# Kernel tuning notes

Hardware: AMD Instinct MI355X
Metric: run time of the kernel (lower is better)

The kernel has to match this reference:

```python
import jax, jax.numpy as jnp
import numpy as np

B, N, IN_DIM, ATT_DIM = 2, 8192, 512, 512


def setup_inputs() -> dict:
    key = jax.random.key(0)
    k1, k2, k3, k4 = jax.random.split(key, 4)
    X = jax.random.normal(k1, (B, N, IN_DIM), dtype=jnp.float32)
    adj = jax.random.uniform(k2, (B, N, N), dtype=jnp.float32)
    mask = jnp.ones((B, N), dtype=jnp.float32)
    # Learned params (torch Linear stores W as (out,in); we store (in,out) for x @ W)
    Wqk = jax.random.normal(k3, (IN_DIM, 2 * ATT_DIM), dtype=jnp.float32) / np.sqrt(IN_DIM)
    Wv = jax.random.normal(k4, (IN_DIM, IN_DIM), dtype=jnp.float32) / np.sqrt(IN_DIM)
    return {"X": X, "adj": adj, "mask": mask, "Wqk": Wqk, "Wv": Wv}


def reference(X, adj, mask, Wqk, Wv):
    # q, k: (B, N, att_dim); v: (B, N, in_dim)
    qk = X @ Wqk
    q, k = jnp.split(qk, 2, axis=-1)
    v = X @ Wv
    att_dim = q.shape[-1]
    inv_scale = 1.0 / jnp.sqrt(jnp.float32(att_dim))
    # Original math: w_i = inv_scale * sum_j adj_ij * m_i * m_j * (q_i . k_j).
    # Since the rank-1 mask factors (m_i m_j), fold m_j into k and m_i into the row
    # score, avoiding a second materialized NxN tensor:
    k_m = k * mask[:, :, None]                       # (B, N, att_dim)
    agg = jnp.einsum("bij,bjd->bid", adj, k_m)       # (B, N, att_dim)
    w = inv_scale * mask * jnp.einsum("bid,bid->bi", q, agg)  # (B, N)
    # softmax over the bag dimension (dim=1), then scale v rows
    L = jax.nn.softmax(w, axis=1)[:, :, None] * v    # (B, N, in_dim)
    return L
```

## Files before the change

kernel.cpp:

```cpp
#include <hip/hip_runtime.h>
#include <math.h>

#define BB 2
#define NN 8192
#define DD 512

static const float INV_SCALE = 0.04419417382415922f;

typedef short s16x8 __attribute__((ext_vector_type(8)));
typedef unsigned short u16x8 __attribute__((ext_vector_type(8)));
typedef float f32x4 __attribute__((ext_vector_type(4)));

#define AS1 __attribute__((address_space(1)))
#define AS3 __attribute__((address_space(3)))

__device__ __forceinline__ unsigned short bfbits(__bf16 h) {
    return __builtin_bit_cast(unsigned short, h);
}

__device__ __forceinline__ void gll16(const void* g, void* l) {
    __builtin_amdgcn_global_load_lds((const AS1 unsigned int*)g, (AS3 unsigned int*)l, 16, 0, 0);
}

__global__ __launch_bounds__(256) void convx_k(
    const float* __restrict__ X, unsigned short* __restrict__ Xhi,
    unsigned short* __restrict__ Xlo)
{
    long i = (long)blockIdx.x * 256 + threadIdx.x;
    float4 x = ((const float4*)X)[i];
    __bf16 h0 = (__bf16)x.x, h1 = (__bf16)x.y, h2 = (__bf16)x.z, h3 = (__bf16)x.w;
    ushort4 hi4 = make_ushort4(bfbits(h0), bfbits(h1), bfbits(h2), bfbits(h3));
    __bf16 l0 = (__bf16)(x.x - (float)h0), l1 = (__bf16)(x.y - (float)h1);
    __bf16 l2 = (__bf16)(x.z - (float)h2), l3 = (__bf16)(x.w - (float)h3);
    ushort4 lo4 = make_ushort4(bfbits(l0), bfbits(l1), bfbits(l2), bfbits(l3));
    ((ushort4*)Xhi)[i] = hi4;
    ((ushort4*)Xlo)[i] = lo4;
}

__global__ __launch_bounds__(256) void convw_k(
    const float* __restrict__ Wqk, const float* __restrict__ Wv,
    unsigned short* __restrict__ QTh, unsigned short* __restrict__ QTl,
    unsigned short* __restrict__ VTh, unsigned short* __restrict__ VTl)
{
    int i = blockIdx.x * 256 + threadIdx.x;
    float val; unsigned short *ph, *pl;
    if (i < 524288) {
        int n = i >> 9, k = i & 511;
        val = Wqk[k * 1024 + n]; ph = QTh + i; pl = QTl + i;
    } else {
        int o = i - 524288; int n = o >> 9, k = o & 511;
        val = Wv[k * 512 + n]; ph = VTh + o; pl = VTl + o;
    }
    __bf16 h = (__bf16)val;
    __bf16 l = (__bf16)(val - (float)h);
    *ph = bfbits(h); *pl = bfbits(l);
}

template <int EPI, int NT>
__global__ __launch_bounds__(256, 2) void mfma_gemm(
    const unsigned short* __restrict__ A0, const unsigned short* __restrict__ A1,
    const unsigned short* __restrict__ B0, const unsigned short* __restrict__ B1,
    float* __restrict__ C,
    float* __restrict__ q, float* __restrict__ km,
    unsigned short* __restrict__ qh, unsigned short* __restrict__ kmh,
    const float* __restrict__ mask, int N, int K)
{
    constexpr int BK = 32;
    constexpr int TILE_SH = 128 * BK;

    __shared__ unsigned short Asm[2 * TILE_SH];
    __shared__ unsigned short Bsm[2 * TILE_SH];

    const int t = threadIdx.x;
    const int wv = t >> 6, lane = t & 63;
    const int wm = wv >> 1, wn = wv & 1;
    const long m0 = blockIdx.x * 128;
    const int n0 = blockIdx.y * 128;

    f32x4 acc[4][4];
#pragma unroll
    for (int i = 0; i < 4; ++i)
#pragma unroll
        for (int j = 0; j < 4; ++j) acc[i][j] = {0.f, 0.f, 0.f, 0.f};

    const int swzcol = ((lane & 3) ^ ((lane >> 2) & 3)) * 16;
    auto stageA16 = [&](int term, int k0, int buf) {
        const unsigned short* Ab = (term < 2) ? A0 : A1;
#pragma unroll
        for (int u = 0; u < 2; ++u) {
            int c = wv * 2 + u;
            int row = c * 16 + (lane >> 2);
            gll16((const char*)Ab + ((m0 + row) * (long)K + k0) * 2 + swzcol,
                  (char*)Asm + buf * (TILE_SH * 2) + c * 1024);
        }
    };
    auto stageB16 = [&](int term, int k0, int buf) {
        const unsigned short* Bb = (NT == 3 && term == 1) ? B1 : B0;
#pragma unroll
        for (int u = 0; u < 2; ++u) {
            int c = wv * 2 + u;
            int row = c * 16 + (lane >> 2);
            gll16((const char*)Bb + ((long)(n0 + row) * K + k0) * 2 + swzcol,
                  (char*)Bsm + buf * (TILE_SH * 2) + c * 1024);
        }
    };

    stageA16(0, 0, 0);
    stageB16(0, 0, 0);
    __syncthreads();

    const int NTILES = NT * (K / BK);
    int cur = 0, term = 0, k0 = 0;
    const int g = lane >> 4;

#pragma unroll 2
    for (int tt = 0; tt < NTILES; ++tt) {
        int k0n = k0 + BK, termn = term;
        if (k0n == K) { k0n = 0; ++termn; }
        const bool hasNext = (tt + 1 < NTILES);

        if (hasNext) {
            stageA16(termn, k0n, cur ^ 1);
            stageB16(termn, k0n, cur ^ 1);
        }

        s16x8 av[4], bv[4];
#pragma unroll
        for (int f = 0; f < 4; ++f) {
            int ra = wm * 64 + f * 16 + (lane & 15);
            int rb = wn * 64 + f * 16 + (lane & 15);
            av[f] = *(const s16x8*)(Asm + cur * TILE_SH + ra * BK + ((g ^ (ra & 3)) << 3));
            bv[f] = *(const s16x8*)(Bsm + cur * TILE_SH + rb * BK + ((g ^ (rb & 3)) << 3));
        }
#pragma unroll
        for (int fm = 0; fm < 4; ++fm)
#pragma unroll
            for (int fn = 0; fn < 4; ++fn)
                acc[fm][fn] = __builtin_amdgcn_mfma_f32_16x16x32_bf16(
                    av[fm], bv[fn], acc[fm][fn], 0, 0, 0);

        __syncthreads();
        cur ^= 1; term = termn; k0 = k0n;
    }

    const long rbase = m0 + wm * 64;
    const int cbase = n0 + wn * 64;

    if constexpr (EPI == 0) {
#pragma unroll
        for (int fm = 0; fm < 4; ++fm) {
            long rb = rbase + fm * 16 + ((lane >> 4) << 2);
#pragma unroll
            for (int fn = 0; fn < 4; ++fn) {
                int c = cbase + fn * 16 + (lane & 15);
#pragma unroll
                for (int j = 0; j < 4; ++j)
                    C[(rb + j) * (long)N + c] = acc[fm][fn][j];
            }
        }
    } else {
        const bool isq = (n0 < 512);
#pragma unroll
        for (int fm = 0; fm < 4; ++fm) {
            long rb = rbase + fm * 16 + ((lane >> 4) << 2);
#pragma unroll
            for (int fn = 0; fn < 4; ++fn) {
                int c = cbase + fn * 16 + (lane & 15);
                if (isq) {
#pragma unroll
                    for (int j = 0; j < 4; ++j) {
                        float val = acc[fm][fn][j];
                        q [(rb + j) * 512L + c] = val;
                        qh[(rb + j) * 512L + c] = bfbits((__bf16)val);
                    }
                } else {
                    int c2 = c - 512;
#pragma unroll
                    for (int j = 0; j < 4; ++j) {
                        float kv = acc[fm][fn][j] * mask[rb + j];
                        km [(rb + j) * 512L + c2] = kv;
                        kmh[(rb + j) * 512L + c2] = bfbits((__bf16)kv);
                    }
                }
            }
        }
    }
}

__global__ __launch_bounds__(256, 4) void sq_gemm(
    const unsigned short* __restrict__ qh,
    const unsigned short* __restrict__ kmh,
    const float* __restrict__ adj,
    float* __restrict__ w)
{
    constexpr int BK = 32;
    constexpr int TILE_SH = 128 * BK;

    __shared__ unsigned short Asm[2 * TILE_SH];
    __shared__ unsigned short Bsm[2 * TILE_SH];

    const int t = threadIdx.x;
    const int wv = t >> 6, lane = t & 63;
    const int wm = wv >> 1, wn = wv & 1;
    const int z = blockIdx.z;
    const long m0 = (long)z * NN + blockIdx.x * 128;
    const int n0 = blockIdx.y * 128;
    const unsigned short* Bz = kmh + (long)z * NN * 512;

    f32x4 acc[4][4];
#pragma unroll
    for (int i = 0; i < 4; ++i)
#pragma unroll
        for (int j = 0; j < 4; ++j) acc[i][j] = {0.f, 0.f, 0.f, 0.f};

    const int swzcol = ((lane & 3) ^ ((lane >> 2) & 3)) * 16;
    auto stageA = [&](int k0, int buf) {
#pragma unroll
        for (int u = 0; u < 2; ++u) {
            int c = wv * 2 + u;
            int row = c * 16 + (lane >> 2);
            gll16((const char*)qh + ((m0 + row) * 512L + k0) * 2 + swzcol,
                  (char*)Asm + buf * (TILE_SH * 2) + c * 1024);
        }
    };
    auto stageB = [&](int k0, int buf) {
#pragma unroll
        for (int u = 0; u < 2; ++u) {
            int c = wv * 2 + u;
            int row = c * 16 + (lane >> 2);
            gll16((const char*)Bz + ((long)(n0 + row) * 512 + k0) * 2 + swzcol,
                  (char*)Bsm + buf * (TILE_SH * 2) + c * 1024);
        }
    };

    stageA(0, 0);
    stageB(0, 0);
    __syncthreads();

    const int g = lane >> 4;
#pragma unroll 2
    for (int tt = 0; tt < 16; ++tt) {
        const int cur = tt & 1;
        const bool hasNext = (tt + 1 < 16);
        if (hasNext) {
            stageA((tt + 1) * BK, cur ^ 1);
            stageB((tt + 1) * BK, cur ^ 1);
        }

        s16x8 av[4], bv[4];
#pragma unroll
        for (int f = 0; f < 4; ++f) {
            int ra = wm * 64 + f * 16 + (lane & 15);
            int rb = wn * 64 + f * 16 + (lane & 15);
            av[f] = *(const s16x8*)(Asm + cur * TILE_SH + ra * BK + ((g ^ (ra & 3)) << 3));
            bv[f] = *(const s16x8*)(Bsm + cur * TILE_SH + rb * BK + ((g ^ (rb & 3)) << 3));
        }
#pragma unroll
        for (int fm = 0; fm < 4; ++fm)
#pragma unroll
            for (int fn = 0; fn < 4; ++fn)
                acc[fm][fn] = __builtin_amdgcn_mfma_f32_16x16x32_bf16(
                    av[fm], bv[fn], acc[fm][fn], 0, 0, 0);

        __syncthreads();
    }

    const float* adjZ = adj + (long)z * NN * NN;
    const int libase = blockIdx.x * 128 + wm * 64;
    const int jbase = n0 + wn * 64;
#pragma unroll
    for (int fm = 0; fm < 4; ++fm) {
#pragma unroll
        for (int j = 0; j < 4; ++j) {
            int li = libase + fm * 16 + ((lane >> 4) << 2) + j;
            const float* ar = adjZ + (long)li * NN + jbase + (lane & 15);
            float s = 0.f;
#pragma unroll
            for (int fn = 0; fn < 4; ++fn)
                s += ar[fn * 16] * acc[fm][fn][j];
            s += __shfl_xor(s, 1); s += __shfl_xor(s, 2);
            s += __shfl_xor(s, 4); s += __shfl_xor(s, 8);
            if ((lane & 15) == 0) atomicAdd(w + (long)z * NN + li, s);
        }
    }
}

__global__ __launch_bounds__(256) void fixup_k(
    float* __restrict__ w, const float* __restrict__ mask)
{
    int i = blockIdx.x * 256 + threadIdx.x;
    w[i] *= INV_SCALE * mask[i];
}

__global__ __launch_bounds__(256) void wmax_k(const float* __restrict__ w,
                                              float* __restrict__ wmax)
{
    const int b = blockIdx.x;
    const float* wr = w + (long)b * NN;
    const int t = threadIdx.x;
    float m = -3.4e38f;
    for (int i = t; i < NN; i += 256) m = fmaxf(m, wr[i]);
#pragma unroll
    for (int o = 32; o > 0; o >>= 1) m = fmaxf(m, __shfl_down(m, o));
    __shared__ float red[4];
    if ((t & 63) == 0) red[t >> 6] = m;
    __syncthreads();
    if (t == 0) wmax[b] = fmaxf(fmaxf(red[0], red[1]), fmaxf(red[2], red[3]));
}

__global__ __launch_bounds__(256) void select_k(
    const float* __restrict__ w, const float* __restrict__ wmax,
    int* __restrict__ count, int* __restrict__ cand)
{
    int i = blockIdx.x * 256 + threadIdx.x;
    int b = i >> 13;
    if (w[i] >= wmax[b] - 15.f) {
        int p = atomicAdd(count, 1);
        if (p < 128) cand[p] = i;
    }
}

__global__ __launch_bounds__(256) void refine_k(
    const float* __restrict__ q, const float* __restrict__ km,
    const float* __restrict__ adj, const int* __restrict__ cand,
    const int* __restrict__ count, float* __restrict__ partial)
{
    int y = blockIdx.y;
    int cnt = *count; if (cnt > 128) cnt = 128;
    if (y >= cnt) return;
    const int row = cand[y];
    const int b = row >> 13, r = row & 8191;
    const int x = blockIdx.x;
    const int t = threadIdx.x, w = t >> 6, l = t & 63;

    const float* qr = q + (long)row * 512 + l * 8;
    const float4 q0 = *(const float4*)qr;
    const float4 q1 = *(const float4*)(qr + 4);
    const float* kmB = km + ((long)b << 13) * 512;
    const float* adjR = adj + (((long)b << 13) + r) * 8192L;

    float acc = 0.f;
    const int jbase = x * 128 + w * 32;
    for (int i = 0; i < 32; ++i) {
        int j = jbase + i;
        const float* kr = kmB + (long)j * 512 + l * 8;
        const float4 k0 = *(const float4*)kr;
        const float4 k1 = *(const float4*)(kr + 4);
        float d = q0.x * k0.x + q0.y * k0.y + q0.z * k0.z + q0.w * k0.w
                + q1.x * k1.x + q1.y * k1.y + q1.z * k1.z + q1.w * k1.w;
#pragma unroll
        for (int o = 32; o > 0; o >>= 1) d += __shfl_down(d, o);
        if (l == 0) acc += adjR[j] * d;
    }
    __shared__ float red[4];
    if (l == 0) red[w] = acc;
    __syncthreads();
    if (t == 0) partial[y * 64 + x] = red[0] + red[1] + red[2] + red[3];
}

__global__ __launch_bounds__(128) void apply_k(
    const int* __restrict__ cand, const int* __restrict__ count,
    const float* __restrict__ partial, const float* __restrict__ mask,
    float* __restrict__ w)
{
    int t = threadIdx.x;
    int cnt = *count; if (cnt > 128) cnt = 128;
    if (t < cnt) {
        float s = 0.f;
        for (int x = 0; x < 64; ++x) s += partial[t * 64 + x];
        int row = cand[t];
        w[row] = s * INV_SCALE * mask[row];
    }
}

__global__ __launch_bounds__(1024) void softmax_k(
    const float* __restrict__ w, float* __restrict__ p)
{
    const int b = blockIdx.x;
    const float* wr = w + (long)b * NN;
    float* pr = p + (long)b * NN;
    const int t = threadIdx.x;
    __shared__ float red[16];
    __shared__ float bmax, bsum;

    float m = -3.4e38f;
    for (int i = t; i < NN; i += 1024) m = fmaxf(m, wr[i]);
#pragma unroll
    for (int o = 32; o > 0; o >>= 1) m = fmaxf(m, __shfl_down(m, o));
    if ((t & 63) == 0) red[t >> 6] = m;
    __syncthreads();
    if (t == 0) {
        float mm = red[0];
        for (int i = 1; i < 16; ++i) mm = fmaxf(mm, red[i]);
        bmax = mm;
    }
    __syncthreads();
    const float M = bmax;

    float s = 0.f;
    for (int i = t; i < NN; i += 1024) s += expf(wr[i] - M);
#pragma unroll
    for (int o = 32; o > 0; o >>= 1) s += __shfl_down(s, o);
    __syncthreads();
    if ((t & 63) == 0) red[t >> 6] = s;
    __syncthreads();
    if (t == 0) {
        float ss = 0.f;
        for (int i = 0; i < 16; ++i) ss += red[i];
        bsum = ss;
    }
    __syncthreads();
    const float invS = 1.f / bsum;
    for (int i = t; i < NN; i += 1024) pr[i] = expf(wr[i] - M) * invS;
}

__global__ __launch_bounds__(256) void scale_k(
    const float* __restrict__ v, const float* __restrict__ p,
    float* __restrict__ out)
{
    const long i = (long)blockIdx.x * 256 + threadIdx.x;
    const int row = (int)(i >> 7);
    const float pv = p[row];
    float4 vv = ((const float4*)v)[i];
    vv.x *= pv; vv.y *= pv; vv.z *= pv; vv.w *= pv;
    ((float4*)out)[i] = vv;
}

extern "C" void kernel_launch(void* const* d_in, const int* in_sizes, int n_in,
                              void* d_out, int out_size, void* d_ws, size_t ws_size,
                              hipStream_t stream)
{
    const float* X    = (const float*)d_in[0];
    const float* adj  = (const float*)d_in[1];
    const float* mask = (const float*)d_in[2];
    const float* Wqk  = (const float*)d_in[3];
    const float* Wv   = (const float*)d_in[4];
    float* out = (float*)d_out;

    char* ws = (char*)d_ws;
    const long SZB = 33554432;
    float* q_buf  = (float*)(ws);
    float* km_buf = (float*)(ws + SZB);
    float* v_buf  = (float*)(ws + 2 * SZB);
    unsigned short* Xhi = (unsigned short*)(ws + 3 * SZB);
    unsigned short* Xlo = Xhi + 8388608;
    unsigned short* qh  = (unsigned short*)(ws + 4 * SZB);
    unsigned short* kmh = qh + 8388608;
    unsigned short* QTh = kmh + 8388608;
    unsigned short* QTl = QTh + 524288;
    unsigned short* VTh = QTl + 524288;
    unsigned short* VTl = VTh + 262144;
    float* w_buf = (float*)(VTl + 262144);
    float* p_buf = w_buf + 16384;
    float* wmax  = p_buf + 16384;
    float* partial = wmax + 64;
    int* count = (int*)(partial + 8192);
    int* cand  = count + 64;

    hipMemsetAsync(count, 0, 4, stream);
    hipMemsetAsync(w_buf, 0, 16384 * 4, stream);

    convx_k<<<8192, 256, 0, stream>>>(X, Xhi, Xlo);
    convw_k<<<3072, 256, 0, stream>>>(Wqk, Wv, QTh, QTl, VTh, VTl);

    mfma_gemm<1, 3><<<dim3(128, 8, 1), 256, 0, stream>>>(
        Xhi, Xlo, QTh, QTl, nullptr, q_buf, km_buf, qh, kmh, mask, 1024, 512);

    mfma_gemm<0, 1><<<dim3(128, 4, 1), 256, 0, stream>>>(
        Xhi, nullptr, VTh, nullptr, v_buf, nullptr, nullptr, nullptr, nullptr,
        nullptr, 512, 512);

    sq_gemm<<<dim3(64, 64, 2), 256, 0, stream>>>(qh, kmh, adj, w_buf);

    fixup_k<<<64, 256, 0, stream>>>(w_buf, mask);

    wmax_k<<<BB, 256, 0, stream>>>(w_buf, wmax);
    select_k<<<64, 256, 0, stream>>>(w_buf, wmax, count, cand);
    refine_k<<<dim3(64, 128, 1), 256, 0, stream>>>(q_buf, km_buf, adj, cand, count, partial);
    apply_k<<<1, 128, 0, stream>>>(cand, count, partial, mask, w_buf);

    softmax_k<<<BB, 1024, 0, stream>>>(w_buf, p_buf);
    scale_k<<<8192, 256, 0, stream>>>(v_buf, p_buf, out);
}
```

Measured before the change: 463.3 us.

## Double GEMM K-tile to 64 with 8-way swizzle and XCD-aware block remap

```diff
diff --git a/kernel.cpp b/kernel.cpp
--- a/kernel.cpp
+++ b/kernel.cpp
@@ -56,6 +56,7 @@
     *ph = bfbits(h); *pl = bfbits(l);
 }
 
+
 template <int EPI, int NT>
 __global__ __launch_bounds__(256, 2) void mfma_gemm(
     const unsigned short* __restrict__ A0, const unsigned short* __restrict__ A1,
@@ -65,7 +66,7 @@
     unsigned short* __restrict__ qh, unsigned short* __restrict__ kmh,
     const float* __restrict__ mask, int N, int K)
 {
-    constexpr int BK = 32;
+    constexpr int BK = 64;
     constexpr int TILE_SH = 128 * BK;
 
     __shared__ unsigned short Asm[2 * TILE_SH];
@@ -83,30 +84,30 @@
 #pragma unroll
         for (int j = 0; j < 4; ++j) acc[i][j] = {0.f, 0.f, 0.f, 0.f};
 
-    const int swzcol = ((lane & 3) ^ ((lane >> 2) & 3)) * 16;
-    auto stageA16 = [&](int term, int k0, int buf) {
+    const int swz = ((lane & 7) ^ (lane >> 3)) << 4;
+    auto stageA = [&](int term, int k0, int buf) {
         const unsigned short* Ab = (term < 2) ? A0 : A1;
 #pragma unroll
-        for (int u = 0; u < 2; ++u) {
-            int c = wv * 2 + u;
-            int row = c * 16 + (lane >> 2);
-            gll16((const char*)Ab + ((m0 + row) * (long)K + k0) * 2 + swzcol,
+        for (int u = 0; u < 4; ++u) {
+            int c = wv * 4 + u;
+            int row = c * 8 + (lane >> 3);
+            gll16((const char*)Ab + ((m0 + row) * (long)K + k0) * 2 + swz,
                   (char*)Asm + buf * (TILE_SH * 2) + c * 1024);
         }
     };
-    auto stageB16 = [&](int term, int k0, int buf) {
+    auto stageB = [&](int term, int k0, int buf) {
         const unsigned short* Bb = (NT == 3 && term == 1) ? B1 : B0;
 #pragma unroll
-        for (int u = 0; u < 2; ++u) {
-            int c = wv * 2 + u;
-            int row = c * 16 + (lane >> 2);
-            gll16((const char*)Bb + ((long)(n0 + row) * K + k0) * 2 + swzcol,
+        for (int u = 0; u < 4; ++u) {
+            int c = wv * 4 + u;
+            int row = c * 8 + (lane >> 3);
+            gll16((const char*)Bb + ((long)(n0 + row) * K + k0) * 2 + swz,
                   (char*)Bsm + buf * (TILE_SH * 2) + c * 1024);
         }
     };
 
-    stageA16(0, 0, 0);
-    stageB16(0, 0, 0);
+    stageA(0, 0, 0);
+    stageB(0, 0, 0);
     __syncthreads();
 
     const int NTILES = NT * (K / BK);
@@ -120,24 +121,29 @@
         const bool hasNext = (tt + 1 < NTILES);
 
         if (hasNext) {
-            stageA16(termn, k0n, cur ^ 1);
-            stageB16(termn, k0n, cur ^ 1);
-        }
-
-        s16x8 av[4], bv[4];
-#pragma unroll
-        for (int f = 0; f < 4; ++f) {
-            int ra = wm * 64 + f * 16 + (lane & 15);
-            int rb = wn * 64 + f * 16 + (lane & 15);
-            av[f] = *(const s16x8*)(Asm + cur * TILE_SH + ra * BK + ((g ^ (ra & 3)) << 3));
-            bv[f] = *(const s16x8*)(Bsm + cur * TILE_SH + rb * BK + ((g ^ (rb & 3)) << 3));
-        }
-#pragma unroll
-        for (int fm = 0; fm < 4; ++fm)
-#pragma unroll
-            for (int fn = 0; fn < 4; ++fn)
-                acc[fm][fn] = __builtin_amdgcn_mfma_f32_16x16x32_bf16(
-                    av[fm], bv[fn], acc[fm][fn], 0, 0, 0);
+            stageA(termn, k0n, cur ^ 1);
+            stageB(termn, k0n, cur ^ 1);
+        }
+
+#pragma unroll
+        for (int ks = 0; ks < 2; ++ks) {
+            s16x8 av[4], bv[4];
+#pragma unroll
+            for (int f = 0; f < 4; ++f) {
+                int ra = wm * 64 + f * 16 + (lane & 15);
+                int rb = wn * 64 + f * 16 + (lane & 15);
+                av[f] = *(const s16x8*)(Asm + cur * TILE_SH + ra * BK
+                         + (((g + ks * 4) ^ (ra & 7)) << 3));
+                bv[f] = *(const s16x8*)(Bsm + cur * TILE_SH + rb * BK
+                         + (((g + ks * 4) ^ (rb & 7)) << 3));
+            }
+#pragma unroll
+            for (int fm = 0; fm < 4; ++fm)
+#pragma unroll
+                for (int fn = 0; fn < 4; ++fn)
+                    acc[fm][fn] = __builtin_amdgcn_mfma_f32_16x16x32_bf16(
+                        av[fm], bv[fn], acc[fm][fn], 0, 0, 0);
+        }
 
         __syncthreads();
         cur ^= 1; term = termn; k0 = k0n;
@@ -187,13 +193,13 @@
     }
 }
 
-__global__ __launch_bounds__(256, 4) void sq_gemm(
+__global__ __launch_bounds__(256, 2) void sq_gemm(
     const unsigned short* __restrict__ qh,
     const unsigned short* __restrict__ kmh,
     const float* __restrict__ adj,
     float* __restrict__ w)
 {
-    constexpr int BK = 32;
+    constexpr int BK = 64;
     constexpr int TILE_SH = 128 * BK;
 
     __shared__ unsigned short Asm[2 * TILE_SH];
@@ -202,9 +208,16 @@
     const int t = threadIdx.x;
     const int wv = t >> 6, lane = t & 63;
     const int wm = wv >> 1, wn = wv & 1;
-    const int z = blockIdx.z;
-    const long m0 = (long)z * NN + blockIdx.x * 128;
-    const int n0 = blockIdx.y * 128;
+
+    const int bid = (int)blockIdx.x;
+    const int xcd = bid & 7, s = bid >> 3;
+    const int z = s >> 9, r = s & 511;
+    const int jj = r & 7, ii = (r >> 3) & 7, jhi = r >> 6;
+    const int i_tile = xcd * 8 + ii;
+    const int j_tile = jhi * 8 + jj;
+
+    const long m0 = (long)z * NN + (long)i_tile * 128;
+    const int n0 = j_tile * 128;
     const unsigned short* Bz = kmh + (long)z * NN * 512;
 
     f32x4 acc[4][4];
@@ -213,22 +226,22 @@
 #pragma unroll
         for (int j = 0; j < 4; ++j) acc[i][j] = {0.f, 0.f, 0.f, 0.f};
 
-    const int swzcol = ((lane & 3) ^ ((lane >> 2) & 3)) * 16;
+    const int swz = ((lane & 7) ^ (lane >> 3)) << 4;
     auto stageA = [&](int k0, int buf) {
 #pragma unroll
-        for (int u = 0; u < 2; ++u) {
-            int c = wv * 2 + u;
-            int row = c * 16 + (lane >> 2);
-            gll16((const char*)qh + ((m0 + row) * 512L + k0) * 2 + swzcol,
+        for (int u = 0; u < 4; ++u) {
+            int c = wv * 4 + u;
+            int row = c * 8 + (lane >> 3);
+            gll16((const char*)qh + ((m0 + row) * 512L + k0) * 2 + swz,
                   (char*)Asm + buf * (TILE_SH * 2) + c * 1024);
         }
     };
     auto stageB = [&](int k0, int buf) {
 #pragma unroll
-        for (int u = 0; u < 2; ++u) {
-            int c = wv * 2 + u;
-            int row = c * 16 + (lane >> 2);
-            gll16((const char*)Bz + ((long)(n0 + row) * 512 + k0) * 2 + swzcol,
+        for (int u = 0; u < 4; ++u) {
+            int c = wv * 4 + u;
+            int row = c * 8 + (lane >> 3);
+            gll16((const char*)Bz + ((long)(n0 + row) * 512 + k0) * 2 + swz,
                   (char*)Bsm + buf * (TILE_SH * 2) + c * 1024);
         }
     };
@@ -239,34 +252,39 @@
 
     const int g = lane >> 4;
 #pragma unroll 2
-    for (int tt = 0; tt < 16; ++tt) {
+    for (int tt = 0; tt < 8; ++tt) {
         const int cur = tt & 1;
-        const bool hasNext = (tt + 1 < 16);
+        const bool hasNext = (tt + 1 < 8);
         if (hasNext) {
             stageA((tt + 1) * BK, cur ^ 1);
             stageB((tt + 1) * BK, cur ^ 1);
         }
 
-        s16x8 av[4], bv[4];
-#pragma unroll
-        for (int f = 0; f < 4; ++f) {
-            int ra = wm * 64 + f * 16 + (lane & 15);
-            int rb = wn * 64 + f * 16 + (lane & 15);
-            av[f] = *(const s16x8*)(Asm + cur * TILE_SH + ra * BK + ((g ^ (ra & 3)) << 3));
-            bv[f] = *(const s16x8*)(Bsm + cur * TILE_SH + rb * BK + ((g ^ (rb & 3)) << 3));
-        }
-#pragma unroll
-        for (int fm = 0; fm < 4; ++fm)
-#pragma unroll
-            for (int fn = 0; fn < 4; ++fn)
-                acc[fm][fn] = __builtin_amdgcn_mfma_f32_16x16x32_bf16(
-                    av[fm], bv[fn], acc[fm][fn], 0, 0, 0);
+#pragma unroll
+        for (int ks = 0; ks < 2; ++ks) {
+            s16x8 av[4], bv[4];
+#pragma unroll
+            for (int f = 0; f < 4; ++f) {
+                int ra = wm * 64 + f * 16 + (lane & 15);
+                int rb = wn * 64 + f * 16 + (lane & 15);
+                av[f] = *(const s16x8*)(Asm + cur * TILE_SH + ra * BK
+                         + (((g + ks * 4) ^ (ra & 7)) << 3));
+                bv[f] = *(const s16x8*)(Bsm + cur * TILE_SH + rb * BK
+                         + (((g + ks * 4) ^ (rb & 7)) << 3));
+            }
+#pragma unroll
+            for (int fm = 0; fm < 4; ++fm)
+#pragma unroll
+                for (int fn = 0; fn < 4; ++fn)
+                    acc[fm][fn] = __builtin_amdgcn_mfma_f32_16x16x32_bf16(
+                        av[fm], bv[fn], acc[fm][fn], 0, 0, 0);
+        }
 
         __syncthreads();
     }
 
     const float* adjZ = adj + (long)z * NN * NN;
-    const int libase = blockIdx.x * 128 + wm * 64;
+    const int libase = i_tile * 128 + wm * 64;
     const int jbase = n0 + wn * 64;
 #pragma unroll
     for (int fm = 0; fm < 4; ++fm) {
@@ -274,13 +292,13 @@
         for (int j = 0; j < 4; ++j) {
             int li = libase + fm * 16 + ((lane >> 4) << 2) + j;
             const float* ar = adjZ + (long)li * NN + jbase + (lane & 15);
-            float s = 0.f;
+            float s2 = 0.f;
 #pragma unroll
             for (int fn = 0; fn < 4; ++fn)
-                s += ar[fn * 16] * acc[fm][fn][j];
-            s += __shfl_xor(s, 1); s += __shfl_xor(s, 2);
-            s += __shfl_xor(s, 4); s += __shfl_xor(s, 8);
-            if ((lane & 15) == 0) atomicAdd(w + (long)z * NN + li, s);
+                s2 += ar[fn * 16] * acc[fm][fn][j];
+            s2 += __shfl_xor(s2, 1); s2 += __shfl_xor(s2, 2);
+            s2 += __shfl_xor(s2, 4); s2 += __shfl_xor(s2, 8);
+            if ((lane & 15) == 0) atomicAdd(w + (long)z * NN + li, s2);
         }
     }
 }
@@ -470,7 +488,7 @@
         Xhi, nullptr, VTh, nullptr, v_buf, nullptr, nullptr, nullptr, nullptr,
         nullptr, 512, 512);
 
-    sq_gemm<<<dim3(64, 64, 2), 256, 0, stream>>>(qh, kmh, adj, w_buf);
+    sq_gemm<<<8192, 256, 0, stream>>>(qh, kmh, adj, w_buf);
 
     fixup_k<<<64, 256, 0, stream>>>(w_buf, mask);
 
```

Measured after the change: 511.5 us. 10.4% more time.
